# Kernel optimization log

Measured on AMD Instinct MI355X. Metric: run time of the kernel, lower is better.

## Reference

```python
import jax, jax.numpy as jnp
import numpy as np

D_IN = 1024
D_OUT = 1024
NUM_HEADS = 16
DIM_HEAD = D_OUT // NUM_HEADS


def setup_inputs() -> dict:
    key = jax.random.key(0)
    ks = jax.random.split(key, 6)
    s = 0.02
    x = jax.random.normal(ks[0], (2, 2048, D_IN), dtype=jnp.float32)
    Wk = jax.random.normal(ks[1], (D_IN, D_OUT), dtype=jnp.float32) * s
    Wq = jax.random.normal(ks[2], (D_IN, D_OUT), dtype=jnp.float32) * s
    Wv = jax.random.normal(ks[3], (D_IN, D_OUT), dtype=jnp.float32) * s
    Wo = jax.random.normal(ks[4], (D_OUT, D_OUT), dtype=jnp.float32) * s
    bo = jax.random.normal(ks[5], (D_OUT,), dtype=jnp.float32) * s
    return {"x": x, "Wk": Wk, "Wq": Wq, "Wv": Wv, "Wo": Wo, "bo": bo}


def reference(x, Wk, Wq, Wv, Wo, bo):
    B, S, _ = x.shape
    # projections -> [B, H, S, Dh]
    def split_heads(t):
        return t.reshape(B, S, NUM_HEADS, DIM_HEAD).transpose(0, 2, 1, 3)
    q = split_heads(x @ Wq)
    k = split_heads(x @ Wk)
    v = split_heads(x @ Wv)
    # NOTE: source uses non-in-place masked_fill whose result is discarded,
    # so NO causal mask is actually applied (faithful reproduction).
    scores = jnp.einsum("bhqd,bhkd->bhqk", q, k) / jnp.sqrt(jnp.float32(DIM_HEAD))
    wgts = jax.nn.softmax(scores, axis=-1)  # dropout = identity (eval mode)
    ctx = jnp.einsum("bhqk,bhkd->bhqd", wgts, v)
    ctx = ctx.transpose(0, 2, 1, 3).reshape(B, S, D_OUT)
    return ctx @ Wo + bo
```

## Files before the change

### kernel.cpp

```cpp
#include <hip/hip_runtime.h>
#include <stdint.h>

typedef short bf16x8 __attribute__((ext_vector_type(8)));
typedef float f32x4  __attribute__((ext_vector_type(4)));
typedef unsigned int u32x4 __attribute__((ext_vector_type(4)));
typedef unsigned int u32x2 __attribute__((ext_vector_type(2)));

__device__ __forceinline__ unsigned short f2bf(float f) {
  unsigned int u = __builtin_bit_cast(unsigned int, f) + 0x8000u;
  return (unsigned short)(u >> 16);
}
__device__ __forceinline__ unsigned int pack2bf(float a, float b) {
  unsigned int ua = __builtin_bit_cast(unsigned int, a) + 0x8000u;
  unsigned int ub = __builtin_bit_cast(unsigned int, b) + 0x8000u;
  return __builtin_amdgcn_perm(ub, ua, 0x07060302);
}

__device__ __forceinline__ void gl2lds16(const void* g, void* l) {
  __builtin_amdgcn_global_load_lds(
      (const __attribute__((address_space(1))) void*)g,
      (__attribute__((address_space(3))) void*)l, 16, 0, 0);
}

template <int N> __device__ __forceinline__ void wait_vmcnt() {
  asm volatile("s_waitcnt vmcnt(%0)" ::"n"(N) : "memory");
}

__global__ __launch_bounds__(256) void cast_x_k(const float* __restrict__ x,
                                                unsigned short* __restrict__ xb) {
  int i = blockIdx.x * 256 + threadIdx.x;
  float4 v = ((const float4*)x)[i];
  u32x2 o;
  o.x = pack2bf(v.x, v.y);
  o.y = pack2bf(v.z, v.w);
  ((u32x2*)xb)[i] = o;
}

__global__ __launch_bounds__(256) void castT_k(
    const float* __restrict__ Wq, const float* __restrict__ Wk,
    const float* __restrict__ Wv, const float* __restrict__ Wo,
    unsigned short* __restrict__ Tq, unsigned short* __restrict__ Tk,
    unsigned short* __restrict__ Tv, unsigned short* __restrict__ To) {
  __shared__ float tile[32][33];
  const int z = blockIdx.z;
  const float* W = (z == 0) ? Wq : (z == 1) ? Wk : (z == 2) ? Wv : Wo;
  unsigned short* T = (z == 0) ? Tq : (z == 1) ? Tk : (z == 2) ? Tv : To;
  const int tx = threadIdx.x, ty = threadIdx.y;
  const int n0 = blockIdx.x * 32, k0 = blockIdx.y * 32;
#pragma unroll
  for (int j = 0; j < 32; j += 8)
    tile[ty + j][tx] = W[(size_t)(k0 + ty + j) * 1024 + n0 + tx];
  __syncthreads();
#pragma unroll
  for (int j = 0; j < 32; j += 8)
    T[(size_t)(n0 + ty + j) * 1024 + k0 + tx] = f2bf(tile[tx][ty + j]);
}

template <int MODE, int TN, int WN, int NTHR>
__global__ __launch_bounds__(NTHR, 2) void gemm_bt_k(const unsigned short* __restrict__ A,
                                                     const unsigned short* __restrict__ B,
                                                     void* __restrict__ C,
                                                     const float* __restrict__ bias,
                                                     int K) {
  constexpr int BN = WN * TN * 16;
  constexpr int ALD = 512 / NTHR;
  constexpr int BLD = BN * 4 / NTHR;
  static_assert(ALD + BLD == 4, "PT must be 4 (vmcnt constants)");
  __shared__ alignas(16) short lA[4][512 * 8];
  __shared__ alignas(16) short lB[4][BN * 4 * 8];
  const int tid = threadIdx.x;
  const int wid = tid >> 6, lane = tid & 63;
  const int l15 = lane & 15, quad = lane >> 4;
  const int waveM = wid / WN, waveN = wid % WN;
  const int bm = blockIdx.y * 128, bn = blockIdx.x * BN;

  f32x4 acc[4][TN];
#pragma unroll
  for (int i = 0; i < 4; ++i)
#pragma unroll
    for (int j = 0; j < TN; ++j) acc[i][j] = (f32x4){0.f, 0.f, 0.f, 0.f};

  auto stage = [&](int kk, short* la, short* lb) {
#pragma unroll
    for (int j = 0; j < ALD; ++j) {
      int c = tid + NTHR * j;
      int row = ((c >> 6) << 4) | (c & 15);
      int ch = (c >> 4) & 3;
      gl2lds16(A + (size_t)(bm + row) * K + kk + ch * 8, &la[(c & ~63) * 8]);
    }
#pragma unroll
    for (int j = 0; j < BLD; ++j) {
      int c = tid + NTHR * j;
      int row = ((c >> 6) << 4) | (c & 15);
      int ch = (c >> 4) & 3;
      gl2lds16(B + (size_t)(bn + row) * K + kk + ch * 8, &lb[(c & ~63) * 8]);
    }
  };

  auto compute = [&](const short* la, const short* lb) {
    bf16x8 af[4], bfr[TN];
#pragma unroll
    for (int i = 0; i < 4; ++i)
      af[i] = *(const bf16x8*)&la[(((waveM * 4 + i) * 64) + lane) * 8];
#pragma unroll
    for (int j = 0; j < TN; ++j)
      bfr[j] = *(const bf16x8*)&lb[(((waveN * TN + j) * 64) + lane) * 8];
    __builtin_amdgcn_s_setprio(1);
#pragma unroll
    for (int i = 0; i < 4; ++i)
#pragma unroll
      for (int j = 0; j < TN; ++j)
        acc[i][j] = __builtin_amdgcn_mfma_f32_16x16x32_bf16(af[i], bfr[j], acc[i][j], 0, 0, 0);
    __builtin_amdgcn_s_setprio(0);
  };

  const int NT = K >> 5;
  short *pa0 = lA[0], *pa1 = lA[1], *pa2 = lA[2], *pa3 = lA[3];
  short *pb0 = lB[0], *pb1 = lB[1], *pb2 = lB[2], *pb3 = lB[3];
  stage(0, pa0, pb0);
  stage(32, pa1, pb1);
#pragma unroll 1
  for (int t = 0; t < NT - 2; ++t) {
    stage((t + 2) * 32, pa2, pb2);
    wait_vmcnt<8>();
    __builtin_amdgcn_sched_barrier(0);
    __builtin_amdgcn_s_barrier();
    __builtin_amdgcn_sched_barrier(0);
    compute(pa0, pb0);
    short* ta = pa0; pa0 = pa1; pa1 = pa2; pa2 = pa3; pa3 = ta;
    short* tb = pb0; pb0 = pb1; pb1 = pb2; pb2 = pb3; pb3 = tb;
  }
  wait_vmcnt<4>();
  __builtin_amdgcn_sched_barrier(0);
  __builtin_amdgcn_s_barrier();
  __builtin_amdgcn_sched_barrier(0);
  compute(pa0, pb0);
  { short* ta = pa0; pa0 = pa1; pa1 = pa2; pa2 = pa3; pa3 = ta;
    short* tb = pb0; pb0 = pb1; pb1 = pb2; pb2 = pb3; pb3 = tb; }
  wait_vmcnt<0>();
  __builtin_amdgcn_sched_barrier(0);
  __builtin_amdgcn_s_barrier();
  __builtin_amdgcn_sched_barrier(0);
  compute(pa0, pb0);

#pragma unroll
  for (int i = 0; i < 4; ++i)
#pragma unroll
    for (int j = 0; j < TN; ++j) {
      int row = bm + waveM * 64 + i * 16 + quad * 4;
      int col = bn + (waveN * TN + j) * 16 + l15;
      if (MODE == 0) {
        unsigned short* Cq = (unsigned short*)C;
        int w = col >> 10, n1 = col & 1023;
        int h = n1 >> 6, d = n1 & 63;
        int b = row >> 11, s = row & 2047;
        int bhh = (b << 4) + h;
        if (w == 2) {
          int g = (i << 2) + quad;
          int ks2 = g >> 3, rem = g & 7;
          int pos = ((ks2 << 2) + (rem & 3)) * 8 + (rem >> 2) * 4;
          u32x2 pk;
          pk.x = pack2bf(acc[i][j][0], acc[i][j][1]);
          pk.y = pack2bf(acc[i][j][2], acc[i][j][3]);
          *(u32x2*)&Cq[(size_t)2 * 4194304 + ((size_t)bhh * 64 + d) * 2048 +
                       (s & ~63) + pos] = pk;
        } else {
          float sc = (w == 0) ? 0.18033688011112042f : 1.0f;
#pragma unroll
          for (int r = 0; r < 4; ++r)
            Cq[(size_t)w * 4194304 + ((size_t)bhh * 2048 + s + r) * 64 + d] =
                f2bf(acc[i][j][r] * sc);
        }
      } else {
#pragma unroll
        for (int r = 0; r < 4; ++r)
          ((float*)C)[(size_t)(row + r) * 1024 + col] = acc[i][j][r] + bias[col];
      }
    }
}

__global__ __launch_bounds__(256, 2) void flash_k(const unsigned short* __restrict__ Qh,
                                                  const unsigned short* __restrict__ Kh,
                                                  const unsigned short* __restrict__ Vt,
                                                  unsigned short* __restrict__ ctxb) {
  constexpr int SL = 2048;
  __shared__ alignas(16) short kt[4][512 * 8];
  __shared__ alignas(16) short vt[4][512 * 8];

  const int tid = threadIdx.x;
  const int wid = tid >> 6, lane = tid & 63;
  const int l15 = lane & 15, quad = lane >> 4;
  const int bid = blockIdx.x;
  const int jj = bid >> 3;
  const int bh = ((bid & 7) << 2) | (jj >> 4);
  const int q0 = (jj & 15) * 128 + wid * 32;

  const unsigned short* Qb = Qh + (size_t)bh * SL * 64;
  const unsigned short* Kb = Kh + (size_t)bh * SL * 64;
  const unsigned short* Vb = Vt + (size_t)bh * 64 * SL;

  bf16x8 qf[2][2];
#pragma unroll
  for (int s = 0; s < 2; ++s)
#pragma unroll
    for (int ks = 0; ks < 2; ++ks)
      qf[s][ks] = *(const bf16x8*)(Qb + (size_t)(q0 + s * 16 + l15) * 64 + ks * 32 + quad * 8);

  f32x4 o[2][4];
  f32x4 rs4[2] = {(f32x4){0.f, 0.f, 0.f, 0.f}, (f32x4){0.f, 0.f, 0.f, 0.f}};
  const f32x4 z4 = (f32x4){0.f, 0.f, 0.f, 0.f};
#pragma unroll
  for (int s = 0; s < 2; ++s)
#pragma unroll
    for (int t = 0; t < 4; ++t) o[s][t] = z4;

  auto stage = [&](int kb, short* ktb, short* vtb) {
#pragma unroll
    for (int j2 = 0; j2 < 2; ++j2) {
      int cc = tid + 256 * j2;
      int row = cc >> 3;
      int ko = (cc & 7) ^ (row & 7);
      gl2lds16(Kb + (size_t)(kb + row) * 64 + ko * 8, &ktb[(cc & ~63) * 8]);
      gl2lds16(Vb + (size_t)row * SL + kb + ko * 8, &vtb[(cc & ~63) * 8]);
    }
  };

  auto compute = [&](const short* ktb, const short* vtb) {
    f32x4 sv[2][4];
    __builtin_amdgcn_s_setprio(1);
#pragma unroll
    for (int t = 0; t < 4; ++t) {
      int key = t * 16 + l15;
      bf16x8 kf0 = *(bf16x8*)&ktb[(key * 8 + (quad ^ (key & 7))) * 8];
      bf16x8 kf1 = *(bf16x8*)&ktb[(key * 8 + ((4 + quad) ^ (key & 7))) * 8];
#pragma unroll
      for (int s = 0; s < 2; ++s) {
        sv[s][t] = __builtin_amdgcn_mfma_f32_16x16x32_bf16(kf0, qf[s][0], z4, 0, 0, 0);
        sv[s][t] = __builtin_amdgcn_mfma_f32_16x16x32_bf16(kf1, qf[s][1], sv[s][t], 0, 0, 0);
      }
    }
    __builtin_amdgcn_s_setprio(0);
    u32x4 pf[2][2];
#pragma unroll
    for (int s = 0; s < 2; ++s)
#pragma unroll
      for (int t = 0; t < 4; ++t) {
        f32x4 p;
#pragma unroll
        for (int r = 0; r < 4; ++r) p[r] = __builtin_amdgcn_exp2f(sv[s][t][r]);
        rs4[s] += p;
        pf[s][t >> 1][(t & 1) * 2 + 0] = pack2bf(p[0], p[1]);
        pf[s][t >> 1][(t & 1) * 2 + 1] = pack2bf(p[2], p[3]);
      }
    __builtin_amdgcn_s_setprio(1);
#pragma unroll
    for (int t = 0; t < 4; ++t) {
      int d = t * 16 + l15;
#pragma unroll
      for (int ks = 0; ks < 2; ++ks) {
        bf16x8 vf = *(bf16x8*)&vtb[(d * 8 + ((ks * 4 + quad) ^ (d & 7))) * 8];
#pragma unroll
        for (int s = 0; s < 2; ++s)
          o[s][t] = __builtin_amdgcn_mfma_f32_16x16x32_bf16(
              vf, __builtin_bit_cast(bf16x8, pf[s][ks]), o[s][t], 0, 0, 0);
      }
    }
    __builtin_amdgcn_s_setprio(0);
  };

  short *k0 = kt[0], *k1 = kt[1], *k2 = kt[2], *k3 = kt[3];
  short *v0 = vt[0], *v1 = vt[1], *v2 = vt[2], *v3 = vt[3];
  stage(0, k0, v0);
  stage(64, k1, v1);
#pragma unroll 1
  for (int t = 0; t < 30; ++t) {
    stage((t + 2) * 64, k2, v2);
    wait_vmcnt<8>();
    __builtin_amdgcn_sched_barrier(0);
    __builtin_amdgcn_s_barrier();
    __builtin_amdgcn_sched_barrier(0);
    compute(k0, v0);
    short* tk = k0; k0 = k1; k1 = k2; k2 = k3; k3 = tk;
    short* tv = v0; v0 = v1; v1 = v2; v2 = v3; v3 = tv;
  }
  wait_vmcnt<4>();
  __builtin_amdgcn_sched_barrier(0);
  __builtin_amdgcn_s_barrier();
  __builtin_amdgcn_sched_barrier(0);
  compute(k0, v0);
  { short* tk = k0; k0 = k1; k1 = k2; k2 = k3; k3 = tk;
    short* tv = v0; v0 = v1; v1 = v2; v2 = v3; v3 = tv; }
  wait_vmcnt<0>();
  __builtin_amdgcn_sched_barrier(0);
  __builtin_amdgcn_s_barrier();
  __builtin_amdgcn_sched_barrier(0);
  compute(k0, v0);

  const int bb = bh >> 4, h = bh & 15;
#pragma unroll
  for (int s = 0; s < 2; ++s) {
    float v = (rs4[s][0] + rs4[s][1]) + (rs4[s][2] + rs4[s][3]);
    v += __shfl_xor(v, 16);
    v += __shfl_xor(v, 32);
    float inv = 1.0f / v;
    int tok = q0 + s * 16 + l15;
    size_t base = ((size_t)(bb * 2048 + tok)) * 1024 + h * 64;
#pragma unroll
    for (int t = 0; t < 4; ++t) {
      u32x2 pk;
      pk.x = pack2bf(o[s][t][0] * inv, o[s][t][1] * inv);
      pk.y = pack2bf(o[s][t][2] * inv, o[s][t][3] * inv);
      *(u32x2*)&ctxb[base + t * 16 + quad * 4] = pk;
    }
  }
}

extern "C" void kernel_launch(void* const* d_in, const int* in_sizes, int n_in,
                              void* d_out, int out_size, void* d_ws, size_t ws_size,
                              hipStream_t stream) {
  const float* x  = (const float*)d_in[0];
  const float* Wk = (const float*)d_in[1];
  const float* Wq = (const float*)d_in[2];
  const float* Wv = (const float*)d_in[3];
  const float* Wo = (const float*)d_in[4];
  const float* bo = (const float*)d_in[5];
  float* out = (float*)d_out;

  char* ws = (char*)d_ws;
  const size_t MB = 1u << 20;
  unsigned short* xb   = (unsigned short*)(ws);
  unsigned short* WqT  = (unsigned short*)(ws + 8  * MB);
  unsigned short* WkT  = (unsigned short*)(ws + 10 * MB);
  unsigned short* WvT  = (unsigned short*)(ws + 12 * MB);
  unsigned short* WoT  = (unsigned short*)(ws + 14 * MB);
  unsigned short* Qh   = (unsigned short*)(ws + 16 * MB);
  unsigned short* ctxb = xb;

  cast_x_k<<<4096, 256, 0, stream>>>(x, xb);
  castT_k<<<dim3(32, 32, 4), dim3(32, 8), 0, stream>>>(Wq, Wk, Wv, Wo, WqT, WkT, WvT, WoT);
  gemm_bt_k<0, 6, 4, 512><<<dim3(8, 32), 512, 0, stream>>>(xb, WqT, Qh, nullptr, 1024);
  flash_k<<<512, 256, 0, stream>>>(Qh, Qh + 4194304, Qh + 2 * 4194304, ctxb);
  gemm_bt_k<1, 4, 2, 256><<<dim3(8, 32), 256, 0, stream>>>(ctxb, WoT, out, bo, 1024);
}
```

Before: 193.2 us.

## Fuse cast kernels, pair flash KV tiles, use hw bf16 pack, retune out GEMM

Merges the x cast and the weight transpose-cast into a single launch to save launch overhead. Restructures the flash attention loop to double-buffer pairs of K/V tiles and issue QK^T for two tiles before softmax/PV, exposing more MFMA ILP at the cost of a full vmcnt(0) wait per iteration. Uses v_cvt_pk_bf16_f32 for packing probabilities. Switches the output projection GEMM to a 512-thread config and generalises vmcnt constants accordingly.

```diff
diff --git a/kernel.cpp b/kernel.cpp
--- a/kernel.cpp
+++ b/kernel.cpp
@@ -15,6 +15,11 @@
   unsigned int ub = __builtin_bit_cast(unsigned int, b) + 0x8000u;
   return __builtin_amdgcn_perm(ub, ua, 0x07060302);
 }
+__device__ __forceinline__ unsigned int cvtpk2bf(float a, float b) {
+  unsigned int r;
+  asm("v_cvt_pk_bf16_f32 %0, %1, %2" : "=v"(r) : "v"(a), "v"(b));
+  return r;
+}
 
 __device__ __forceinline__ void gl2lds16(const void* g, void* l) {
   __builtin_amdgcn_global_load_lds(
@@ -26,34 +31,37 @@
   asm volatile("s_waitcnt vmcnt(%0)" ::"n"(N) : "memory");
 }
 
-__global__ __launch_bounds__(256) void cast_x_k(const float* __restrict__ x,
-                                                unsigned short* __restrict__ xb) {
-  int i = blockIdx.x * 256 + threadIdx.x;
-  float4 v = ((const float4*)x)[i];
-  u32x2 o;
-  o.x = pack2bf(v.x, v.y);
-  o.y = pack2bf(v.z, v.w);
-  ((u32x2*)xb)[i] = o;
-}
-
-__global__ __launch_bounds__(256) void castT_k(
+__global__ __launch_bounds__(256) void cast_fused_k(
+    const float* __restrict__ x, unsigned short* __restrict__ xb,
     const float* __restrict__ Wq, const float* __restrict__ Wk,
     const float* __restrict__ Wv, const float* __restrict__ Wo,
     unsigned short* __restrict__ Tq, unsigned short* __restrict__ Tk,
     unsigned short* __restrict__ Tv, unsigned short* __restrict__ To) {
   __shared__ float tile[32][33];
-  const int z = blockIdx.z;
-  const float* W = (z == 0) ? Wq : (z == 1) ? Wk : (z == 2) ? Wv : Wo;
-  unsigned short* T = (z == 0) ? Tq : (z == 1) ? Tk : (z == 2) ? Tv : To;
-  const int tx = threadIdx.x, ty = threadIdx.y;
-  const int n0 = blockIdx.x * 32, k0 = blockIdx.y * 32;
-#pragma unroll
-  for (int j = 0; j < 32; j += 8)
-    tile[ty + j][tx] = W[(size_t)(k0 + ty + j) * 1024 + n0 + tx];
-  __syncthreads();
-#pragma unroll
-  for (int j = 0; j < 32; j += 8)
-    T[(size_t)(n0 + ty + j) * 1024 + k0 + tx] = f2bf(tile[tx][ty + j]);
+  const int tid = threadIdx.x;
+  const int bid = blockIdx.x;
+  if (bid < 4096) {
+    int i = bid * 256 + tid;
+    float4 v = ((const float4*)x)[i];
+    u32x2 o;
+    o.x = pack2bf(v.x, v.y);
+    o.y = pack2bf(v.z, v.w);
+    ((u32x2*)xb)[i] = o;
+  } else {
+    const int bb = bid - 4096;
+    const int z = bb >> 10, rem = bb & 1023;
+    const float* W = (z == 0) ? Wq : (z == 1) ? Wk : (z == 2) ? Wv : Wo;
+    unsigned short* T = (z == 0) ? Tq : (z == 1) ? Tk : (z == 2) ? Tv : To;
+    const int tx = tid & 31, ty = tid >> 5;
+    const int n0 = (rem & 31) * 32, k0 = (rem >> 5) * 32;
+#pragma unroll
+    for (int j = 0; j < 32; j += 8)
+      tile[ty + j][tx] = W[(size_t)(k0 + ty + j) * 1024 + n0 + tx];
+    __syncthreads();
+#pragma unroll
+    for (int j = 0; j < 32; j += 8)
+      T[(size_t)(n0 + ty + j) * 1024 + k0 + tx] = f2bf(tile[tx][ty + j]);
+  }
 }
 
 template <int MODE, int TN, int WN, int NTHR>
@@ -65,7 +73,7 @@
   constexpr int BN = WN * TN * 16;
   constexpr int ALD = 512 / NTHR;
   constexpr int BLD = BN * 4 / NTHR;
-  static_assert(ALD + BLD == 4, "PT must be 4 (vmcnt constants)");
+  constexpr int PT = ALD + BLD;
   __shared__ alignas(16) short lA[4][512 * 8];
   __shared__ alignas(16) short lB[4][BN * 4 * 8];
   const int tid = threadIdx.x;
@@ -122,7 +130,7 @@
 #pragma unroll 1
   for (int t = 0; t < NT - 2; ++t) {
     stage((t + 2) * 32, pa2, pb2);
-    wait_vmcnt<8>();
+    wait_vmcnt<2 * PT>();
     __builtin_amdgcn_sched_barrier(0);
     __builtin_amdgcn_s_barrier();
     __builtin_amdgcn_sched_barrier(0);
@@ -130,7 +138,7 @@
     short* ta = pa0; pa0 = pa1; pa1 = pa2; pa2 = pa3; pa3 = ta;
     short* tb = pb0; pb0 = pb1; pb1 = pb2; pb2 = pb3; pb3 = tb;
   }
-  wait_vmcnt<4>();
+  wait_vmcnt<PT>();
   __builtin_amdgcn_sched_barrier(0);
   __builtin_amdgcn_s_barrier();
   __builtin_amdgcn_sched_barrier(0);
@@ -225,8 +233,7 @@
     }
   };
 
-  auto compute = [&](const short* ktb, const short* vtb) {
-    f32x4 sv[2][4];
+  auto computeQK = [&](const short* ktb, f32x4 (&sv)[2][4]) {
     __builtin_amdgcn_s_setprio(1);
 #pragma unroll
     for (int t = 0; t < 4; ++t) {
@@ -240,6 +247,9 @@
       }
     }
     __builtin_amdgcn_s_setprio(0);
+  };
+
+  auto computeSMPV = [&](const short* vtb, f32x4 (&sv)[2][4]) {
     u32x4 pf[2][2];
 #pragma unroll
     for (int s = 0; s < 2; ++s)
@@ -249,8 +259,8 @@
 #pragma unroll
         for (int r = 0; r < 4; ++r) p[r] = __builtin_amdgcn_exp2f(sv[s][t][r]);
         rs4[s] += p;
-        pf[s][t >> 1][(t & 1) * 2 + 0] = pack2bf(p[0], p[1]);
-        pf[s][t >> 1][(t & 1) * 2 + 1] = pack2bf(p[2], p[3]);
+        pf[s][t >> 1][(t & 1) * 2 + 0] = cvtpk2bf(p[0], p[1]);
+        pf[s][t >> 1][(t & 1) * 2 + 1] = cvtpk2bf(p[2], p[3]);
       }
     __builtin_amdgcn_s_setprio(1);
 #pragma unroll
@@ -268,33 +278,29 @@
     __builtin_amdgcn_s_setprio(0);
   };
 
-  short *k0 = kt[0], *k1 = kt[1], *k2 = kt[2], *k3 = kt[3];
-  short *v0 = vt[0], *v1 = vt[1], *v2 = vt[2], *v3 = vt[3];
-  stage(0, k0, v0);
-  stage(64, k1, v1);
+  short *kA0 = kt[0], *kA1 = kt[1], *kB0 = kt[2], *kB1 = kt[3];
+  short *vA0 = vt[0], *vA1 = vt[1], *vB0 = vt[2], *vB1 = vt[3];
+  stage(0, kA0, vA0);
+  stage(64, kA1, vA1);
 #pragma unroll 1
-  for (int t = 0; t < 30; ++t) {
-    stage((t + 2) * 64, k2, v2);
-    wait_vmcnt<8>();
+  for (int i2 = 0; i2 < 16; ++i2) {
+    wait_vmcnt<0>();
     __builtin_amdgcn_sched_barrier(0);
     __builtin_amdgcn_s_barrier();
     __builtin_amdgcn_sched_barrier(0);
-    compute(k0, v0);
-    short* tk = k0; k0 = k1; k1 = k2; k2 = k3; k3 = tk;
-    short* tv = v0; v0 = v1; v1 = v2; v2 = v3; v3 = tv;
+    if (i2 < 15) {
+      stage((2 * i2 + 2) * 64, kB0, vB0);
+      stage((2 * i2 + 3) * 64, kB1, vB1);
+    }
+    f32x4 sv0[2][4], sv1[2][4];
+    computeQK(kA0, sv0);
+    computeQK(kA1, sv1);
+    computeSMPV(vA0, sv0);
+    computeSMPV(vA1, sv1);
+    short* t;
+    t = kA0; kA0 = kB0; kB0 = t;  t = kA1; kA1 = kB1; kB1 = t;
+    t = vA0; vA0 = vB0; vB0 = t;  t = vA1; vA1 = vB1; vB1 = t;
   }
-  wait_vmcnt<4>();
-  __builtin_amdgcn_sched_barrier(0);
-  __builtin_amdgcn_s_barrier();
-  __builtin_amdgcn_sched_barrier(0);
-  compute(k0, v0);
-  { short* tk = k0; k0 = k1; k1 = k2; k2 = k3; k3 = tk;
-    short* tv = v0; v0 = v1; v1 = v2; v2 = v3; v3 = tv; }
-  wait_vmcnt<0>();
-  __builtin_amdgcn_sched_barrier(0);
-  __builtin_amdgcn_s_barrier();
-  __builtin_amdgcn_sched_barrier(0);
-  compute(k0, v0);
 
   const int bb = bh >> 4, h = bh & 15;
 #pragma unroll
@@ -336,9 +342,8 @@
   unsigned short* Qh   = (unsigned short*)(ws + 16 * MB);
   unsigned short* ctxb = xb;
 
-  cast_x_k<<<4096, 256, 0, stream>>>(x, xb);
-  castT_k<<<dim3(32, 32, 4), dim3(32, 8), 0, stream>>>(Wq, Wk, Wv, Wo, WqT, WkT, WvT, WoT);
+  cast_fused_k<<<8192, 256, 0, stream>>>(x, xb, Wq, Wk, Wv, Wo, WqT, WkT, WvT, WoT);
   gemm_bt_k<0, 6, 4, 512><<<dim3(8, 32), 512, 0, stream>>>(xb, WqT, Qh, nullptr, 1024);
   flash_k<<<512, 256, 0, stream>>>(Qh, Qh + 4194304, Qh + 2 * 4194304, ctxb);
-  gemm_bt_k<1, 4, 2, 256><<<dim3(8, 32), 256, 0, stream>>>(ctxb, WoT, out, bo, 1024);
-}
+  gemm_bt_k<1, 2, 4, 512><<<dim3(8, 32), 512, 0, stream>>>(ctxb, WoT, out, bo, 1024);
+}
```

Result: faster. 185.8 us (-3.8%).
